# Performance work log

Hardware: AMD Instinct MI355X
Metric: run time of the kernel (lower is better)

The kernel has to match this reference:

```python
import jax, jax.numpy as jnp
import numpy as np

THRESHOLD = 0.5

def setup_inputs() -> dict:
    key = jax.random.key(0)
    ks = jax.random.split(key, 7)
    dim, hidden = 1024, 4096
    x = jax.random.normal(ks[0], (4, 4096, dim), dtype=jnp.float32)
    # router: Linear(dim, 1)
    W_r = jax.random.normal(ks[1], (dim, 1), dtype=jnp.float32) / np.sqrt(dim)
    b_r = jnp.zeros((1,), dtype=jnp.float32)
    # MLP: Linear(dim, hidden) -> ReLU -> Linear(hidden, dim)
    W1 = jax.random.normal(ks[2], (dim, hidden), dtype=jnp.float32) / np.sqrt(dim)
    b1 = jnp.zeros((hidden,), dtype=jnp.float32)
    W2 = jax.random.normal(ks[3], (hidden, dim), dtype=jnp.float32) / np.sqrt(hidden)
    b2 = jnp.zeros((dim,), dtype=jnp.float32)
    return {"x": x, "W_r": W_r, "b_r": b_r, "W1": W1, "b1": b1, "W2": W2, "b2": b2}

def reference(x, W_r, b_r, W1, b1, W2, b2):
    # router logits per token: [B, S]
    logits = (jnp.einsum('bsd,do->bso', x, W_r) + b_r)[..., 0]
    probs = jax.nn.sigmoid(logits)
    mask = probs > THRESHOLD  # [B, S] bool
    # dense equivalent of gather-MLP-scatter: compute MLP everywhere, select per token
    h = jax.nn.relu(jnp.einsum('bsd,dh->bsh', x, W1) + b1)
    processed = jnp.einsum('bsh,hd->bsd', h, W2) + b2
    output = jnp.where(mask[..., None], processed, x)
    frac = jnp.mean(mask.astype(jnp.float32))
    return (output, frac)
```

## Files before the change

kernel.cpp:

```cpp
#include <hip/hip_runtime.h>
#include <hip/hip_bf16.h>

#define TOKENS 16384
#define DIM 1024
#define HID 4096

typedef __attribute__((ext_vector_type(8))) short short8;
typedef __attribute__((ext_vector_type(4))) float f32x4;

__device__ __forceinline__ unsigned short f2bf(float f) {
  union { float f; unsigned int u; } v; v.f = f;
  unsigned int r = v.u + 0x7fffu + ((v.u >> 16) & 1u);
  return (unsigned short)(r >> 16);
}

__device__ __forceinline__ void async16(const void* g, void* lds) {
  __builtin_amdgcn_global_load_lds((const __attribute__((address_space(1))) void*)g,
                                   (__attribute__((address_space(3))) void*)lds, 16, 0, 0);
}

__global__ __launch_bounds__(256) void router_kernel(
    const float* __restrict__ x, const float* __restrict__ Wr, const float* __restrict__ br,
    float* __restrict__ out, unsigned short* __restrict__ xb,
    int* __restrict__ idx, int* __restrict__ counter)
{
  int wid = threadIdx.x >> 6, lane = threadIdx.x & 63;
  int token = blockIdx.x * 4 + wid;
  const float4* xr  = (const float4*)(x + (size_t)token * DIM);
  const float4* wr4 = (const float4*)Wr;
  float4* outr = (float4*)(out + (size_t)token * DIM);
  ushort4* xbr = (ushort4*)(xb + (size_t)token * DIM);
  double s = 0.0;
#pragma unroll
  for (int j = 0; j < 4; ++j) {
    float4 v = xr[lane + 64 * j];
    float4 w = wr4[lane + 64 * j];
    s += (double)v.x * w.x + (double)v.y * w.y + (double)v.z * w.z + (double)v.w * w.w;
    outr[lane + 64 * j] = v;
    ushort4 u;
    u.x = f2bf(v.x); u.y = f2bf(v.y); u.z = f2bf(v.z); u.w = f2bf(v.w);
    xbr[lane + 64 * j] = u;
  }
#pragma unroll
  for (int off = 32; off > 0; off >>= 1) s += __shfl_down(s, off);
  if (lane == 0) {
    float logit = (float)s + br[0];
    if (logit > 0.0f) {
      int p = atomicAdd(counter, 1);
      idx[p] = token;
    }
  }
}

__global__ __launch_bounds__(256) void transpose_cast_kernel(
    const float* __restrict__ W, unsigned short* __restrict__ Wt, int R, int C)
{
  __shared__ float tile[32][33];
  int tx = threadIdx.x & 31, ty = threadIdx.x >> 5;
  int c0 = blockIdx.x * 32, r0 = blockIdx.y * 32;
#pragma unroll
  for (int i = 0; i < 32; i += 8)
    tile[ty + i][tx] = W[(size_t)(r0 + ty + i) * C + (c0 + tx)];
  __syncthreads();
#pragma unroll
  for (int i = 0; i < 32; i += 8)
    Wt[(size_t)(c0 + ty + i) * R + (r0 + tx)] = f2bf(tile[tx][ty + i]);
}

__global__ void frac_kernel(const int* __restrict__ counter, float* __restrict__ fr)
{
  fr[0] = (float)(*counter) * (1.0f / (float)TOKENS);
}

template<int N, int K, bool FIRST>
__global__ __launch_bounds__(256) void gemm_kernel(
    const unsigned short* __restrict__ A, const unsigned short* __restrict__ Bt,
    const float* __restrict__ bias, const int* __restrict__ idxp,
    const int* __restrict__ counter,
    unsigned short* __restrict__ Hout, float* __restrict__ Cout)
{
  int cnt = *counter;
  int row0 = blockIdx.y * 128;
  if (row0 >= cnt) return;
  int col0 = blockIdx.x * 128;

  __shared__ unsigned short As[128 * 32];
  __shared__ unsigned short Bs[128 * 32];
  __shared__ int rowIdx[128];

  int tid = threadIdx.x, wid = tid >> 6, lane = tid & 63;
  if (tid < 128) rowIdx[tid] = idxp[row0 + tid];
  __syncthreads();

  int sRow0 = wid * 16 + (lane >> 2);
  int sRow1 = 64 + sRow0;
  int chunk = (lane & 3) * 8;
  int ar0 = FIRST ? rowIdx[sRow0] : (row0 + sRow0);
  int ar1 = FIRST ? rowIdx[sRow1] : (row0 + sRow1);
  const unsigned short* gA0 = A + (size_t)ar0 * K + chunk;
  const unsigned short* gA1 = A + (size_t)ar1 * K + chunk;
  const unsigned short* gB0 = Bt + (size_t)(col0 + sRow0) * K + chunk;
  const unsigned short* gB1 = Bt + (size_t)(col0 + sRow1) * K + chunk;
  unsigned short* lA0 = As + (size_t)(wid * 16) * 32;
  unsigned short* lA1 = As + (size_t)(64 + wid * 16) * 32;
  unsigned short* lB0 = Bs + (size_t)(wid * 16) * 32;
  unsigned short* lB1 = Bs + (size_t)(64 + wid * 16) * 32;

  f32x4 acc[4][4];
#pragma unroll
  for (int i = 0; i < 4; ++i)
#pragma unroll
    for (int j = 0; j < 4; ++j) acc[i][j] = (f32x4){0.f, 0.f, 0.f, 0.f};

  int wr = (wid >> 1) * 64, wc = (wid & 1) * 64;
  int frow = lane & 15, khalf = lane >> 4;

  for (int k0 = 0; k0 < K; k0 += 32) {
    async16(gA0 + k0, lA0);
    async16(gA1 + k0, lA1);
    async16(gB0 + k0, lB0);
    async16(gB1 + k0, lB1);
    __syncthreads();
    short8 af[4], bfr[4];
#pragma unroll
    for (int mi = 0; mi < 4; ++mi)
      af[mi] = *(const short8*)&As[(size_t)(wr + mi * 16 + frow) * 32 + khalf * 8];
#pragma unroll
    for (int ni = 0; ni < 4; ++ni)
      bfr[ni] = *(const short8*)&Bs[(size_t)(wc + ni * 16 + frow) * 32 + khalf * 8];
#pragma unroll
    for (int mi = 0; mi < 4; ++mi)
#pragma unroll
      for (int ni = 0; ni < 4; ++ni)
        acc[mi][ni] = __builtin_amdgcn_mfma_f32_16x16x32_bf16(af[mi], bfr[ni], acc[mi][ni], 0, 0, 0);
    __syncthreads();
  }

  int cl = lane & 15, rq = lane >> 4;
#pragma unroll
  for (int mi = 0; mi < 4; ++mi) {
#pragma unroll
    for (int ni = 0; ni < 4; ++ni) {
      int col = col0 + wc + ni * 16 + cl;
      float bv = bias[col];
#pragma unroll
      for (int r = 0; r < 4; ++r) {
        int rloc = wr + mi * 16 + rq * 4 + r;
        int grow = row0 + rloc;
        float val = acc[mi][ni][r] + bv;
        if (FIRST) {
          val = val > 0.f ? val : 0.f;
          Hout[(size_t)grow * N + col] = f2bf(val);
        } else if (grow < cnt) {
          int tok = rowIdx[rloc];
          Cout[(size_t)tok * DIM + col] = val;
        }
      }
    }
  }
}

extern "C" void kernel_launch(void* const* d_in, const int* in_sizes, int n_in,
                              void* d_out, int out_size, void* d_ws, size_t ws_size,
                              hipStream_t stream)
{
  const float* x  = (const float*)d_in[0];
  const float* Wr = (const float*)d_in[1];
  const float* br = (const float*)d_in[2];
  const float* W1 = (const float*)d_in[3];
  const float* b1 = (const float*)d_in[4];
  const float* W2 = (const float*)d_in[5];
  const float* b2 = (const float*)d_in[6];
  float* out = (float*)d_out;

  char* ws = (char*)d_ws;
  int* counter        = (int*)ws;
  int* idx            = (int*)(ws + 256);
  unsigned short* xb  = (unsigned short*)(ws + (1ull  << 20));
  unsigned short* W1T = (unsigned short*)(ws + (34ull << 20));
  unsigned short* W2T = (unsigned short*)(ws + (44ull << 20));
  unsigned short* h   = (unsigned short*)(ws + (54ull << 20));

  hipMemsetAsync(ws, 0, 256 + TOKENS * 4, stream);

  router_kernel<<<TOKENS / 4, 256, 0, stream>>>(x, Wr, br, out, xb, idx, counter);
  transpose_cast_kernel<<<dim3(HID / 32, DIM / 32), 256, 0, stream>>>(W1, W1T, DIM, HID);
  transpose_cast_kernel<<<dim3(DIM / 32, HID / 32), 256, 0, stream>>>(W2, W2T, HID, DIM);
  frac_kernel<<<1, 1, 0, stream>>>(counter, out + (size_t)TOKENS * DIM);

  gemm_kernel<HID, DIM, true><<<dim3(HID / 128, TOKENS / 128), 256, 0, stream>>>(
      xb, W1T, b1, idx, counter, h, nullptr);
  gemm_kernel<DIM, HID, false><<<dim3(DIM / 128, TOKENS / 128), 256, 0, stream>>>(
      h, W2T, b2, idx, counter, nullptr, out);
}
```

Baseline: 434.0 us.

## Write x or bf16 copy selectively, batch router atomics, XCD-swizzle GEMM tiles

The router now processes 16 tokens per block. It writes the fp32 passthrough only for unselected tokens and the bf16 copy only for selected ones, which cuts global writes. Selection flags are gathered in LDS and one atomic per block appends the indices, replacing one atomic per token. The GEMM grids are flattened and remapped so that consecutive tiles land on the same XCD, which should improve L2 reuse. Index order within a block stays deterministic, and the early-exit logic now depends on the swizzled row index.

```diff
diff --git a/kernel.cpp b/kernel.cpp
--- a/kernel.cpp
+++ b/kernel.cpp
@@ -24,31 +24,53 @@
     float* __restrict__ out, unsigned short* __restrict__ xb,
     int* __restrict__ idx, int* __restrict__ counter)
 {
+  __shared__ unsigned char selLds[16];
   int wid = threadIdx.x >> 6, lane = threadIdx.x & 63;
-  int token = blockIdx.x * 4 + wid;
-  const float4* xr  = (const float4*)(x + (size_t)token * DIM);
   const float4* wr4 = (const float4*)Wr;
-  float4* outr = (float4*)(out + (size_t)token * DIM);
-  ushort4* xbr = (ushort4*)(xb + (size_t)token * DIM);
-  double s = 0.0;
-#pragma unroll
-  for (int j = 0; j < 4; ++j) {
-    float4 v = xr[lane + 64 * j];
-    float4 w = wr4[lane + 64 * j];
-    s += (double)v.x * w.x + (double)v.y * w.y + (double)v.z * w.z + (double)v.w * w.w;
-    outr[lane + 64 * j] = v;
-    ushort4 u;
-    u.x = f2bf(v.x); u.y = f2bf(v.y); u.z = f2bf(v.z); u.w = f2bf(v.w);
-    xbr[lane + 64 * j] = u;
-  }
-#pragma unroll
-  for (int off = 32; off > 0; off >>= 1) s += __shfl_down(s, off);
-  if (lane == 0) {
-    float logit = (float)s + br[0];
-    if (logit > 0.0f) {
-      int p = atomicAdd(counter, 1);
-      idx[p] = token;
+  float4 w[4];
+#pragma unroll
+  for (int j = 0; j < 4; ++j) w[j] = wr4[lane + 64 * j];
+  float b0 = br[0];
+
+#pragma unroll
+  for (int t = 0; t < 4; ++t) {
+    int token = blockIdx.x * 16 + wid * 4 + t;
+    const float4* xr = (const float4*)(x + (size_t)token * DIM);
+    float4 v[4];
+#pragma unroll
+    for (int j = 0; j < 4; ++j) v[j] = xr[lane + 64 * j];
+    double s = 0.0;
+#pragma unroll
+    for (int j = 0; j < 4; ++j)
+      s += (double)v[j].x * w[j].x + (double)v[j].y * w[j].y +
+           (double)v[j].z * w[j].z + (double)v[j].w * w[j].w;
+#pragma unroll
+    for (int off = 32; off > 0; off >>= 1) s += __shfl_xor(s, off);
+    bool sel = ((float)s + b0) > 0.0f;
+    if (sel) {
+      ushort4* xbr = (ushort4*)(xb + (size_t)token * DIM);
+#pragma unroll
+      for (int j = 0; j < 4; ++j) {
+        ushort4 u;
+        u.x = f2bf(v[j].x); u.y = f2bf(v[j].y); u.z = f2bf(v[j].z); u.w = f2bf(v[j].w);
+        xbr[lane + 64 * j] = u;
+      }
+    } else {
+      float4* outr = (float4*)(out + (size_t)token * DIM);
+#pragma unroll
+      for (int j = 0; j < 4; ++j) outr[lane + 64 * j] = v[j];
     }
+    if (lane == 0) selLds[wid * 4 + t] = sel ? 1 : 0;
+  }
+  __syncthreads();
+  if (threadIdx.x == 0) {
+    int cnt = 0;
+#pragma unroll
+    for (int i = 0; i < 16; ++i) cnt += selLds[i];
+    int p = atomicAdd(counter, cnt);
+#pragma unroll
+    for (int i = 0; i < 16; ++i)
+      if (selLds[i]) idx[p++] = blockIdx.x * 16 + i;
   }
 }
 
@@ -79,10 +101,19 @@
     const int* __restrict__ counter,
     unsigned short* __restrict__ Hout, float* __restrict__ Cout)
 {
+  constexpr int MT = TOKENS / 128;
+  constexpr int NWG = (N / 128) * MT;
+  constexpr int q = NWG / 8, r = NWG % 8;
+  int wg = blockIdx.x;
+  int xcd = wg & 7, lin = wg >> 3;
+  int swz = (xcd < r ? xcd * (q + 1) : r * (q + 1) + (xcd - r) * q) + lin;
+  int colb = swz / MT;
+  int rowb = swz % MT;
+
   int cnt = *counter;
-  int row0 = blockIdx.y * 128;
+  int row0 = rowb * 128;
   if (row0 >= cnt) return;
-  int col0 = blockIdx.x * 128;
+  int col0 = colb * 128;
 
   __shared__ unsigned short As[128 * 32];
   __shared__ unsigned short Bs[128 * 32];
@@ -144,10 +175,10 @@
       int col = col0 + wc + ni * 16 + cl;
       float bv = bias[col];
 #pragma unroll
-      for (int r = 0; r < 4; ++r) {
-        int rloc = wr + mi * 16 + rq * 4 + r;
+      for (int r2 = 0; r2 < 4; ++r2) {
+        int rloc = wr + mi * 16 + rq * 4 + r2;
         int grow = row0 + rloc;
-        float val = acc[mi][ni][r] + bv;
+        float val = acc[mi][ni][r2] + bv;
         if (FIRST) {
           val = val > 0.f ? val : 0.f;
           Hout[(size_t)grow * N + col] = f2bf(val);
@@ -183,13 +214,13 @@
 
   hipMemsetAsync(ws, 0, 256 + TOKENS * 4, stream);
 
-  router_kernel<<<TOKENS / 4, 256, 0, stream>>>(x, Wr, br, out, xb, idx, counter);
+  router_kernel<<<TOKENS / 16, 256, 0, stream>>>(x, Wr, br, out, xb, idx, counter);
   transpose_cast_kernel<<<dim3(HID / 32, DIM / 32), 256, 0, stream>>>(W1, W1T, DIM, HID);
   transpose_cast_kernel<<<dim3(DIM / 32, HID / 32), 256, 0, stream>>>(W2, W2T, HID, DIM);
   frac_kernel<<<1, 1, 0, stream>>>(counter, out + (size_t)TOKENS * DIM);
 
-  gemm_kernel<HID, DIM, true><<<dim3(HID / 128, TOKENS / 128), 256, 0, stream>>>(
+  gemm_kernel<HID, DIM, true><<<(HID / 128) * (TOKENS / 128), 256, 0, stream>>>(
       xb, W1T, b1, idx, counter, h, nullptr);
-  gemm_kernel<DIM, HID, false><<<dim3(DIM / 128, TOKENS / 128), 256, 0, stream>>>(
+  gemm_kernel<DIM, HID, false><<<(DIM / 128) * (TOKENS / 128), 256, 0, stream>>>(
       h, W2T, b2, idx, counter, nullptr, out);
 }
```

Result: faster. 383.7 us (-11.6%).
